# Performance work log

Hardware: AMD Instinct MI355X
Metric: run time of the kernel (lower is better)

The kernel has to match this reference:

```python
import jax, jax.numpy as jnp
import numpy as np

B, L, DM = 1, 512, 768
DS, DC, EX = 64, 4, 2
DI = EX * DM            # d_inner = 1536
DR = DM // 16           # dt_rank = 48


def setup_inputs() -> dict:
    key = jax.random.key(0)
    ks = jax.random.split(key, 12)
    s = 0.02
    inp = {
        "x": jax.random.normal(ks[0], (B, L, DM), dtype=jnp.float32),
        "ln_w": jnp.ones((DM,), jnp.float32),
        "ln_b": jnp.zeros((DM,), jnp.float32),
        "in_proj_w": jax.random.normal(ks[1], (2 * DI, DM), jnp.float32) * s,
        "conv_w": jax.random.normal(ks[2], (DI, 1, DC), jnp.float32) * s,
        "conv_b": jnp.zeros((DI,), jnp.float32),
        "x_proj_w": jax.random.normal(ks[3], (DR + 2 * DS, DI), jnp.float32) * s,
        "dt_proj_w": jax.random.normal(ks[4], (DI, DR), jnp.float32) * s,
        "dt_proj_b": jax.random.normal(ks[5], (DI,), jnp.float32) * s,
        "A_log": jnp.log(jnp.broadcast_to(jnp.arange(1, DS + 1, dtype=jnp.float32), (DI, DS))),
        "D": jnp.ones((DI,), jnp.float32),
        "out_proj_w": jax.random.normal(ks[6], (DM, DI), jnp.float32) * s,
    }
    return inp


def _layernorm(x, w, b, eps=1e-5):
    mu = jnp.mean(x, axis=-1, keepdims=True)
    var = jnp.mean((x - mu) ** 2, axis=-1, keepdims=True)
    return (x - mu) * jax.lax.rsqrt(var + eps) * w + b


def _causal_depthwise_conv(x, w, b):
    # x: [B, L, DI] -> conv over time, depthwise, causal (left pad DC-1)
    xc = jnp.transpose(x, (0, 2, 1))  # [B, DI, L]
    y = jax.lax.conv_general_dilated(
        xc, w, window_strides=(1,), padding=[(DC - 1, 0)],
        dimension_numbers=("NCH", "OIH", "NCH"), feature_group_count=DI)
    y = y + b[None, :, None]
    return jnp.transpose(y, (0, 2, 1))  # [B, L, DI]


def _selective_scan(deltaA, deltaB_u, C):
    # deltaA, deltaB_u: [B, L, DI, DS]; C: [B, L, DS]
    dA = jnp.transpose(deltaA, (1, 0, 2, 3))
    dBu = jnp.transpose(deltaB_u, (1, 0, 2, 3))
    Ct = jnp.transpose(C, (1, 0, 2))
    s0 = jnp.zeros(deltaA.shape[:1] + deltaA.shape[2:], deltaA.dtype).transpose(0, 1, 2)
    s0 = jnp.zeros((deltaA.shape[0], deltaA.shape[2], deltaA.shape[3]), deltaA.dtype)

    def step(s, inp):
        dA_t, dBu_t, C_t = inp
        s = dA_t * s + dBu_t                      # [B, DI, DS]
        y = jnp.einsum("bdn,bn->bd", s, C_t)      # [B, DI]
        return s, y

    _, ys = jax.lax.scan(step, s0, (dA, dBu, Ct))
    return jnp.transpose(ys, (1, 0, 2))           # [B, L, DI]


def reference(x, ln_w, ln_b, in_proj_w, conv_w, conv_b, x_proj_w,
              dt_proj_w, dt_proj_b, A_log, D, out_proj_w):
    residual = x
    h = _layernorm(x, ln_w, ln_b)
    xz = jnp.einsum("bld,ed->ble", h, in_proj_w)  # [B, L, 2*DI]
    x_in, z = jnp.split(xz, 2, axis=-1)
    x_in = jax.nn.silu(_causal_depthwise_conv(x_in, conv_w, conv_b))
    x_dbl = jnp.einsum("bld,ed->ble", x_in, x_proj_w)  # [B, L, DR+2*DS]
    dt, Bm, Cm = jnp.split(x_dbl, [DR, DR + DS], axis=-1)
    dt = jax.nn.softplus(jnp.einsum("blr,dr->bld", dt, dt_proj_w) + dt_proj_b)  # [B,L,DI]
    A = -jnp.exp(A_log)                                 # [DI, DS]
    deltaA = jnp.exp(dt[..., None] * A)                 # [B, L, DI, DS]
    deltaB_u = dt[..., None] * Bm[:, :, None, :] * x_in[..., None]
    y = _selective_scan(deltaA, deltaB_u, Cm)           # [B, L, DI]
    y = y + x_in * D
    y = y * jax.nn.silu(z)
    out = jnp.einsum("bld,ed->ble", y, out_proj_w)      # [B, L, DM]
    return residual + out
```

## Files before the change

### kernel.cpp

```cpp
#include <hip/hip_runtime.h>
#include <hip/hip_bf16.h>
#include <math.h>

#define L_SEQ 512
#define DM 768
#define DI 1536
#define DS 64
#define DC 4
#define DR 48
#define NXD 176
#define NC 8
#define TC 64

typedef __attribute__((ext_vector_type(8))) short short8;
typedef __attribute__((ext_vector_type(4))) float float4v;

#define NWI (2 * DI * DM)
#define NWX (NXD * DI)
#define NWDT (DI * DR)
#define NWO (DM * DI)
#define NXZ (L_SEQ * 2 * DI)
#define NXDBL (L_SEQ * NXD)
#define NXR (L_SEQ * DM)

#define B_LN 512
#define B_WI (NWI / 1024)
#define B_WX (NWX / 1024)
#define B_WDT (NWDT / 1024)
#define B_WO (NWO / 1024)
#define PREP_GRID (B_LN + B_WI + B_WX + B_WDT + B_WO)

__device__ __forceinline__ float bp_add(float p, int addr) {
  return p + __int_as_float(__builtin_amdgcn_ds_bpermute(addr, __float_as_int(p)));
}
__device__ __forceinline__ float lane_read(float v, int t) {
  return __int_as_float(__builtin_amdgcn_readlane(__float_as_int(v), t));
}
__device__ __forceinline__ short f2bf(float v) {
  __hip_bfloat16 h = __float2bfloat16(v);
  return *reinterpret_cast<short*>(&h);
}
__device__ __forceinline__ short8 cvt8f(const float* p, bool valid) {
  float4 u = *(const float4*)(p);
  float4 v = *(const float4*)(p + 4);
  short8 r;
  r[0] = f2bf(u.x); r[1] = f2bf(u.y); r[2] = f2bf(u.z); r[3] = f2bf(u.w);
  r[4] = f2bf(v.x); r[5] = f2bf(v.y); r[6] = f2bf(v.z); r[7] = f2bf(v.w);
  if (!valid) r = (short8)0;
  return r;
}

__device__ __forceinline__ void cvt_blk(const float* __restrict__ s,
                                        short* __restrict__ d, int b) {
  int i = b * 1024 + threadIdx.x * 4;
  float4 v = *(const float4*)(s + i);
  short4 o; o.x = f2bf(v.x); o.y = f2bf(v.y); o.z = f2bf(v.z); o.w = f2bf(v.w);
  *(short4*)(d + i) = o;
}
__global__ __launch_bounds__(256) void prep(
    const float* __restrict__ x, const float* __restrict__ lnw,
    const float* __restrict__ lnb, short* __restrict__ h,
    const float* __restrict__ wi, short* __restrict__ wib,
    const float* __restrict__ wx, short* __restrict__ wxb,
    const float* __restrict__ wdt, short* __restrict__ wdtb,
    const float* __restrict__ wo, short* __restrict__ wob) {
  int b = blockIdx.x;
  if (b < B_LN) {
    int l = b, tid = threadIdx.x;
    const float* xr = x + l * DM;
    float s = 0.f, s2 = 0.f;
    for (int i = tid; i < DM; i += 256) { float t = xr[i]; s += t; s2 += t * t; }
#pragma unroll
    for (int off = 32; off; off >>= 1) { s += __shfl_xor(s, off); s2 += __shfl_xor(s2, off); }
    __shared__ float ls[4], ls2[4];
    int wid = tid >> 6, lane = tid & 63;
    if (lane == 0) { ls[wid] = s; ls2[wid] = s2; }
    __syncthreads();
    s = ls[0] + ls[1] + ls[2] + ls[3];
    s2 = ls2[0] + ls2[1] + ls2[2] + ls2[3];
    float mean = s * (1.f / DM);
    float var = s2 * (1.f / DM) - mean * mean;
    float rstd = rsqrtf(var + 1e-5f);
    for (int i = tid; i < DM; i += 256)
      h[l * DM + i] = f2bf((xr[i] - mean) * rstd * lnw[i] + lnb[i]);
    return;
  }
  b -= B_LN;
  if (b < B_WI) { cvt_blk(wi, wib, b); return; }
  b -= B_WI;
  if (b < B_WX) { cvt_blk(wx, wxb, b); return; }
  b -= B_WX;
  if (b < B_WDT) { cvt_blk(wdt, wdtb, b); return; }
  b -= B_WDT;
  cvt_blk(wo, wob, b);
}

__global__ __launch_bounds__(256) void gemm_bf16(const short* __restrict__ A, int lda,
                                                 const short* __restrict__ B,
                                                 float* __restrict__ C,
                                                 int N, int K,
                                                 const float* __restrict__ res,
                                                 int mode) {
  int lane = threadIdx.x & 63, w = threadIdx.x >> 6;
  int fr = lane & 15, koff = (lane >> 4) * 8;
  int mbase = blockIdx.y * 64 + (w & 1) * 32;
  int nbase = blockIdx.x * 64 + (w >> 1) * 32;
  int kchunk = K / gridDim.z;
  int kbeg = blockIdx.z * kchunk;
  int nr0 = nbase + fr;      if (nr0 > N - 1) nr0 = N - 1;
  int nr1 = nbase + 16 + fr; if (nr1 > N - 1) nr1 = N - 1;
  const short* pA0 = A + (size_t)(mbase + fr) * lda + koff + kbeg;
  const short* pA1 = pA0 + (size_t)16 * lda;
  const short* pB0 = B + (size_t)nr0 * K + koff + kbeg;
  const short* pB1 = B + (size_t)nr1 * K + koff + kbeg;
  float4v acc00 = (float4v){0.f,0.f,0.f,0.f}, acc01 = acc00;
  float4v acc10 = acc00, acc11 = acc00;
  short8 a0A = *(const short8*)(pA0);      short8 a1A = *(const short8*)(pA1);
  short8 b0A = *(const short8*)(pB0);      short8 b1A = *(const short8*)(pB1);
  short8 a0B = *(const short8*)(pA0 + 32); short8 a1B = *(const short8*)(pA1 + 32);
  short8 b0B = *(const short8*)(pB0 + 32); short8 b1B = *(const short8*)(pB1 + 32);
  for (int k0 = 0; k0 < kchunk; k0 += 64) {
    short8 ca0 = a0A, ca1 = a1A, cb0 = b0A, cb1 = b1A;
    short8 da0 = a0B, da1 = a1B, db0 = b0B, db1 = b1B;
    int nA = k0 + 64; if (nA >= kchunk) nA = 0;
    int nB = k0 + 96; if (nB >= kchunk) nB = 32;
    a0A = *(const short8*)(pA0 + nA); a1A = *(const short8*)(pA1 + nA);
    b0A = *(const short8*)(pB0 + nA); b1A = *(const short8*)(pB1 + nA);
    a0B = *(const short8*)(pA0 + nB); a1B = *(const short8*)(pA1 + nB);
    b0B = *(const short8*)(pB0 + nB); b1B = *(const short8*)(pB1 + nB);
    acc00 = __builtin_amdgcn_mfma_f32_16x16x32_bf16(ca0, cb0, acc00, 0, 0, 0);
    acc01 = __builtin_amdgcn_mfma_f32_16x16x32_bf16(ca0, cb1, acc01, 0, 0, 0);
    acc10 = __builtin_amdgcn_mfma_f32_16x16x32_bf16(ca1, cb0, acc10, 0, 0, 0);
    acc11 = __builtin_amdgcn_mfma_f32_16x16x32_bf16(ca1, cb1, acc11, 0, 0, 0);
    acc00 = __builtin_amdgcn_mfma_f32_16x16x32_bf16(da0, db0, acc00, 0, 0, 0);
    acc01 = __builtin_amdgcn_mfma_f32_16x16x32_bf16(da0, db1, acc01, 0, 0, 0);
    acc10 = __builtin_amdgcn_mfma_f32_16x16x32_bf16(da1, db0, acc10, 0, 0, 0);
    acc11 = __builtin_amdgcn_mfma_f32_16x16x32_bf16(da1, db1, acc11, 0, 0, 0);
  }
  float* Cz = C + (size_t)blockIdx.z * (size_t)L_SEQ * (size_t)N;
  int col0 = nbase + fr, col1 = nbase + 16 + fr;
  int rb = mbase + (lane >> 4) * 4;
#pragma unroll
  for (int r = 0; r < 4; ++r) {
    size_t o00 = (size_t)(rb + r) * N;
    size_t o10 = (size_t)(rb + 16 + r) * N;
    if (col0 < N) {
      float v0 = acc00[r], v1 = acc10[r];
      if (mode == 2) { v0 += res[o00 + col0]; v1 += res[o10 + col0]; }
      Cz[o00 + col0] = v0; Cz[o10 + col0] = v1;
    }
    if (col1 < N) {
      float v0 = acc01[r], v1 = acc11[r];
      if (mode == 2) { v0 += res[o00 + col1]; v1 += res[o10 + col1]; }
      Cz[o00 + col1] = v0; Cz[o10 + col1] = v1;
    }
  }
}

__global__ __launch_bounds__(256) void reduce_add(const float* __restrict__ part,
                                                  int MN, int splitk,
                                                  float* __restrict__ out) {
  int i = blockIdx.x * 256 + threadIdx.x;
  if (i >= MN) return;
  float a = 0.f;
  for (int z = 0; z < splitk; ++z) a += part[(size_t)z * MN + i];
  out[i] = a;
}

__global__ __launch_bounds__(256) void dtp_gemm(const float* __restrict__ Axd,
                                                const short* __restrict__ Bw,
                                                float* __restrict__ dt,
                                                const float* __restrict__ bias) {
  int lane = threadIdx.x & 63, w = threadIdx.x >> 6;
  int fr = lane & 15, koff = (lane >> 4) * 8;
  int mbase = blockIdx.y * 64 + (w & 1) * 32;
  int nbase = blockIdx.x * 64 + (w >> 1) * 32;
  const float* pA0 = Axd + (size_t)(mbase + fr) * NXD;
  const float* pA1 = pA0 + (size_t)16 * NXD;
  const short* pB0 = Bw + (size_t)(nbase + fr) * DR;
  const short* pB1 = Bw + (size_t)(nbase + 16 + fr) * DR;
  float4v acc00 = (float4v){0.f,0.f,0.f,0.f}, acc01 = acc00;
  float4v acc10 = acc00, acc11 = acc00;
#pragma unroll
  for (int k0 = 0; k0 < 64; k0 += 32) {
    bool valid = (k0 + koff) < DR;
    int off = valid ? k0 + koff : 0;
    short8 a0 = cvt8f(pA0 + off, valid);
    short8 a1 = cvt8f(pA1 + off, valid);
    short8 b0 = *(const short8*)(pB0 + off);
    short8 b1 = *(const short8*)(pB1 + off);
    if (!valid) { b0 = (short8)0; b1 = (short8)0; }
    acc00 = __builtin_amdgcn_mfma_f32_16x16x32_bf16(a0, b0, acc00, 0, 0, 0);
    acc01 = __builtin_amdgcn_mfma_f32_16x16x32_bf16(a0, b1, acc01, 0, 0, 0);
    acc10 = __builtin_amdgcn_mfma_f32_16x16x32_bf16(a1, b0, acc10, 0, 0, 0);
    acc11 = __builtin_amdgcn_mfma_f32_16x16x32_bf16(a1, b1, acc11, 0, 0, 0);
  }
  int col0 = nbase + fr, col1 = nbase + 16 + fr;
  float bi0 = bias[col0], bi1 = bias[col1];
  int rb = mbase + (lane >> 4) * 4;
#pragma unroll
  for (int r = 0; r < 4; ++r) {
    float v0 = acc00[r] + bi0, v1 = acc01[r] + bi1;
    float v2 = acc10[r] + bi0, v3 = acc11[r] + bi1;
    v0 = (v0 > 20.f) ? v0 : log1pf(__expf(v0));
    v1 = (v1 > 20.f) ? v1 : log1pf(__expf(v1));
    v2 = (v2 > 20.f) ? v2 : log1pf(__expf(v2));
    v3 = (v3 > 20.f) ? v3 : log1pf(__expf(v3));
    dt[(size_t)(rb + r) * DI + col0] = v0;
    dt[(size_t)(rb + r) * DI + col1] = v1;
    dt[(size_t)(rb + 16 + r) * DI + col0] = v2;
    dt[(size_t)(rb + 16 + r) * DI + col1] = v3;
  }
}

__global__ __launch_bounds__(256) void conv_silu_kernel(const float* __restrict__ xz,
                                                        const float* __restrict__ cw,
                                                        const float* __restrict__ cb,
                                                        float* __restrict__ xc,
                                                        short* __restrict__ xcb) {
  int idx = blockIdx.x * 256 + threadIdx.x;
  if (idx >= L_SEQ * DI) return;
  int l = idx / DI, d = idx - l * DI;
  float acc = cb[d];
#pragma unroll
  for (int j = 0; j < DC; ++j) {
    int ll = l - (DC - 1) + j;
    if (ll >= 0) acc = fmaf(xz[(size_t)ll * (2 * DI) + d], cw[d * DC + j], acc);
  }
  float sig = 1.f / (1.f + __expf(-acc));
  float v = acc * sig;
  xc[idx] = v;
  xcb[idx] = f2bf(v);
}

__global__ __launch_bounds__(256) void scan_p1(const float* __restrict__ dt,
                                               const float* __restrict__ xc,
                                               const float* __restrict__ xdbl,
                                               const float* __restrict__ A_log,
                                               float* __restrict__ send,
                                               float* __restrict__ dts) {
  int lane = threadIdx.x & 63;
  int wid = threadIdx.x >> 6;
  int pair = blockIdx.x * 4 + wid;
  int c = __builtin_amdgcn_readfirstlane(pair / DI);
  int d = __builtin_amdgcn_readfirstlane(pair - (pair / DI) * DI);
  float A = -__expf(A_log[(size_t)d * DS + lane]);
  int l0 = c * TC;
  float dtv = dt[(size_t)(l0 + lane) * DI + d];
  float xv  = xc[(size_t)(l0 + lane) * DI + d];
  const float* pB = xdbl + (size_t)l0 * NXD + DR + lane;
  float s = 0.f;
#pragma unroll 8
  for (int t = 0; t < TC; ++t) {
    float dt_c = lane_read(dtv, t);
    float x_c  = lane_read(xv, t);
    float B_c  = pB[(size_t)t * NXD];
    float dA = __expf(dt_c * A);
    s = fmaf(dA, s, dt_c * x_c * B_c);
  }
  float dsum = dtv;
  dsum = bp_add(dsum, (lane ^ 1) << 2);  dsum = bp_add(dsum, (lane ^ 2) << 2);
  dsum = bp_add(dsum, (lane ^ 4) << 2);  dsum = bp_add(dsum, (lane ^ 8) << 2);
  dsum = bp_add(dsum, (lane ^ 16) << 2); dsum = bp_add(dsum, (lane ^ 32) << 2);
  send[((size_t)c * DI + d) * DS + lane] = s;
  if (lane == 0) dts[c * DI + d] = dsum;
}

__global__ __launch_bounds__(256) void scan_p2(const float* __restrict__ send,
                                               const float* __restrict__ dts,
                                               const float* __restrict__ A_log,
                                               float* __restrict__ sinit) {
  int lane = threadIdx.x & 63;
  int wid = threadIdx.x >> 6;
  int d = __builtin_amdgcn_readfirstlane(blockIdx.x * 4 + wid);
  float A = -__expf(A_log[(size_t)d * DS + lane]);
  float s = 0.f;
  for (int c = 1; c < NC; ++c) {
    float P = __expf(A * dts[(c - 1) * DI + d]);
    s = fmaf(P, s, send[((size_t)(c - 1) * DI + d) * DS + lane]);
    sinit[((size_t)c * DI + d) * DS + lane] = s;
  }
}

__global__ __launch_bounds__(256) void scan_p3(const float* __restrict__ dt,
                                               const float* __restrict__ xc,
                                               const float* __restrict__ xdbl,
                                               const float* __restrict__ A_log,
                                               const float* __restrict__ Dv,
                                               const float* __restrict__ xz,
                                               const float* __restrict__ sinit,
                                               short* __restrict__ y) {
  __shared__ float Pb[4][16][66];
  int lane = threadIdx.x & 63;
  int wid = threadIdx.x >> 6;
  int pair = blockIdx.x * 4 + wid;
  int c = __builtin_amdgcn_readfirstlane(pair / DI);
  int d = __builtin_amdgcn_readfirstlane(pair - (pair / DI) * DI);
  float A = -__expf(A_log[(size_t)d * DS + lane]);
  float Dd = Dv[d];
  int l0 = c * TC;
  float dtv = dt[(size_t)(l0 + lane) * DI + d];
  float xv  = xc[(size_t)(l0 + lane) * DI + d];
  float zv  = xz[(size_t)(l0 + lane) * (2 * DI) + DI + d];
  float s = (c == 0) ? 0.f : sinit[((size_t)c * DI + d) * DS + lane];
  const float* pB = xdbl + (size_t)l0 * NXD + DR + lane;
  float yv = 0.f;
#pragma unroll
  for (int sb = 0; sb < 4; ++sb) {
    float P[16];
#pragma unroll
    for (int j = 0; j < 16; ++j) {
      int t = sb * 16 + j;
      float dt_c = lane_read(dtv, t);
      float x_c  = lane_read(xv, t);
      float B_c  = pB[(size_t)t * NXD];
      float C_c  = pB[(size_t)t * NXD + DS];
      float dA = __expf(dt_c * A);
      s = fmaf(dA, s, dt_c * x_c * B_c);
      P[j] = s * C_c;
    }
#pragma unroll
    for (int j = 0; j < 16; ++j) Pb[wid][j][lane] = P[j];
    int t4 = lane >> 2, q = lane & 3;
    const float* row = &Pb[wid][t4][q * 16];
    float part = 0.f;
#pragma unroll
    for (int k = 0; k < 8; ++k) {
      float2 v2 = *(const float2*)(row + 2 * k);
      part += v2.x + v2.y;
    }
    part = bp_add(part, (lane ^ 1) << 2);
    part = bp_add(part, (lane ^ 2) << 2);
    float got = __int_as_float(
        __builtin_amdgcn_ds_bpermute((lane & 15) << 4, __float_as_int(part)));
    yv = ((lane >> 4) == sb) ? got : yv;
  }
  float sig = 1.f / (1.f + __expf(-zv));
  y[(size_t)(l0 + lane) * DI + d] = f2bf((yv + xv * Dd) * (zv * sig));
}

extern "C" void kernel_launch(void* const* d_in, const int* in_sizes, int n_in,
                              void* d_out, int out_size, void* d_ws, size_t ws_size,
                              hipStream_t stream) {
  const float* x         = (const float*)d_in[0];
  const float* ln_w      = (const float*)d_in[1];
  const float* ln_b      = (const float*)d_in[2];
  const float* in_proj_w = (const float*)d_in[3];
  const float* conv_w    = (const float*)d_in[4];
  const float* conv_b    = (const float*)d_in[5];
  const float* x_proj_w  = (const float*)d_in[6];
  const float* dt_proj_w = (const float*)d_in[7];
  const float* dt_proj_b = (const float*)d_in[8];
  const float* A_log     = (const float*)d_in[9];
  const float* Dv        = (const float*)d_in[10];
  const float* out_proj_w= (const float*)d_in[11];
  float* out = (float*)d_out;

  float* ws = (float*)d_ws;
  float* xz    = ws;
  float* xconv = xz + NXZ;
  float* xdbl  = xconv + 786432;
  float* dtb   = xdbl + NXDBL;
  float* send  = dtb + 786432;
  float* dts   = send + 688128;
  float* sinit = dts + 10752;
  float* part2 = sinit + 786432;
  float* fend  = part2 + 720896;
  short* h_bf   = (short*)fend;
  short* wi_bf  = h_bf + NXR;
  short* wx_bf  = wi_bf + NWI;
  short* wdt_bf = wx_bf + NWX;
  short* wo_bf  = wdt_bf + NWDT;
  short* xc_bf  = wo_bf + NWO;
  short* y_bf   = xc_bf + (L_SEQ * DI);

  prep<<<PREP_GRID, 256, 0, stream>>>(x, ln_w, ln_b, h_bf,
                                      in_proj_w, wi_bf, x_proj_w, wx_bf,
                                      dt_proj_w, wdt_bf, out_proj_w, wo_bf);

  gemm_bf16<<<dim3(2 * DI / 64, L_SEQ / 64, 1), 256, 0, stream>>>(
      h_bf, DM, wi_bf, xz, 2 * DI, DM, nullptr, 0);

  conv_silu_kernel<<<(L_SEQ * DI) / 256, 256, 0, stream>>>(xz, conv_w, conv_b,
                                                           xconv, xc_bf);

  gemm_bf16<<<dim3((NXD + 63) / 64, L_SEQ / 64, 8), 256, 0, stream>>>(
      xc_bf, DI, wx_bf, part2, NXD, DI, nullptr, 0);
  reduce_add<<<(NXDBL + 255) / 256, 256, 0, stream>>>(part2, NXDBL, 8, xdbl);

  dtp_gemm<<<dim3(DI / 64, L_SEQ / 64), 256, 0, stream>>>(
      xdbl, wdt_bf, dtb, dt_proj_b);

  scan_p1<<<((NC - 1) * DI) / 4, 256, 0, stream>>>(dtb, xconv, xdbl, A_log, send, dts);
  scan_p2<<<DI / 4, 256, 0, stream>>>(send, dts, A_log, sinit);
  scan_p3<<<(NC * DI) / 4, 256, 0, stream>>>(dtb, xconv, xdbl, A_log, Dv, xz, sinit, y_bf);

  gemm_bf16<<<dim3(DM / 64, L_SEQ / 64, 1), 256, 0, stream>>>(
      y_bf, DI, wo_bf, out, DM, DI, x, 2);
}
```

Baseline: 212.4 us.

## Fuse all stages into one cooperative persistent kernel with grid syncs

Replaces the chain of separate kernel launches (prep, three GEMMs, conv, reduce, dt projection, three scan phases) with one cooperative kernel of 512 blocks that runs each stage in turn, separated by grid-wide barriers. The split-K x_proj GEMM now accumulates straight into a zeroed xdbl buffer with atomic adds, so the separate partial buffer and reduce kernel are gone. The aim is to remove launch gaps and the extra partial-sum traffic. In exchange, stages that used more than 512 blocks now loop over work, several stages leave most blocks idle, grid.sync adds its own barrier cost, and atomic accumulation makes the float sums order-dependent.

```diff
diff --git a/kernel.cpp b/kernel.cpp
--- a/kernel.cpp
+++ b/kernel.cpp
@@ -1,6 +1,9 @@
 #include <hip/hip_runtime.h>
+#include <hip/hip_cooperative_groups.h>
 #include <hip/hip_bf16.h>
 #include <math.h>
+
+namespace cg = cooperative_groups;
 
 #define L_SEQ 512
 #define DM 768
@@ -23,12 +26,22 @@
 #define NXDBL (L_SEQ * NXD)
 #define NXR (L_SEQ * DM)
 
-#define B_LN 512
-#define B_WI (NWI / 1024)
-#define B_WX (NWX / 1024)
-#define B_WDT (NWDT / 1024)
-#define B_WO (NWO / 1024)
-#define PREP_GRID (B_LN + B_WI + B_WX + B_WDT + B_WO)
+#define J_LN 512
+#define J_WI (NWI / 1024)
+#define J_WX (NWX / 1024)
+#define J_WDT (NWDT / 1024)
+#define J_WO (NWO / 1024)
+#define J_ZXD (NXDBL / 1024)
+#define NJOBS (J_LN + J_WI + J_WX + J_WDT + J_WO + J_ZXD)
+
+#define GRID_BLOCKS 512
+
+struct Params {
+  const float *x, *lnw, *lnb, *wi, *conv_w, *conv_b, *wx, *wdt, *dt_b, *A_log, *Dv, *wo;
+  float *out;
+  float *xz, *xconv, *xdbl, *dtb, *send, *dts, *sinit;
+  short *h_bf, *wi_bf, *wx_bf, *wdt_bf, *wo_bf, *xc_bf, *y_bf;
+};
 
 __device__ __forceinline__ float bp_add(float p, int addr) {
   return p + __int_as_float(__builtin_amdgcn_ds_bpermute(addr, __float_as_int(p)));
@@ -49,7 +62,9 @@
   if (!valid) r = (short8)0;
   return r;
 }
-
+__device__ __forceinline__ void atomic_addf(float* p, float v) {
+  __hip_atomic_fetch_add(p, v, __ATOMIC_RELAXED, __HIP_MEMORY_SCOPE_AGENT);
+}
 __device__ __forceinline__ void cvt_blk(const float* __restrict__ s,
                                         short* __restrict__ d, int b) {
   int i = b * 1024 + threadIdx.x * 4;
@@ -57,62 +72,22 @@
   short4 o; o.x = f2bf(v.x); o.y = f2bf(v.y); o.z = f2bf(v.z); o.w = f2bf(v.w);
   *(short4*)(d + i) = o;
 }
-__global__ __launch_bounds__(256) void prep(
-    const float* __restrict__ x, const float* __restrict__ lnw,
-    const float* __restrict__ lnb, short* __restrict__ h,
-    const float* __restrict__ wi, short* __restrict__ wib,
-    const float* __restrict__ wx, short* __restrict__ wxb,
-    const float* __restrict__ wdt, short* __restrict__ wdtb,
-    const float* __restrict__ wo, short* __restrict__ wob) {
-  int b = blockIdx.x;
-  if (b < B_LN) {
-    int l = b, tid = threadIdx.x;
-    const float* xr = x + l * DM;
-    float s = 0.f, s2 = 0.f;
-    for (int i = tid; i < DM; i += 256) { float t = xr[i]; s += t; s2 += t * t; }
-#pragma unroll
-    for (int off = 32; off; off >>= 1) { s += __shfl_xor(s, off); s2 += __shfl_xor(s2, off); }
-    __shared__ float ls[4], ls2[4];
-    int wid = tid >> 6, lane = tid & 63;
-    if (lane == 0) { ls[wid] = s; ls2[wid] = s2; }
-    __syncthreads();
-    s = ls[0] + ls[1] + ls[2] + ls[3];
-    s2 = ls2[0] + ls2[1] + ls2[2] + ls2[3];
-    float mean = s * (1.f / DM);
-    float var = s2 * (1.f / DM) - mean * mean;
-    float rstd = rsqrtf(var + 1e-5f);
-    for (int i = tid; i < DM; i += 256)
-      h[l * DM + i] = f2bf((xr[i] - mean) * rstd * lnw[i] + lnb[i]);
-    return;
-  }
-  b -= B_LN;
-  if (b < B_WI) { cvt_blk(wi, wib, b); return; }
-  b -= B_WI;
-  if (b < B_WX) { cvt_blk(wx, wxb, b); return; }
-  b -= B_WX;
-  if (b < B_WDT) { cvt_blk(wdt, wdtb, b); return; }
-  b -= B_WDT;
-  cvt_blk(wo, wob, b);
-}
-
-__global__ __launch_bounds__(256) void gemm_bf16(const short* __restrict__ A, int lda,
-                                                 const short* __restrict__ B,
-                                                 float* __restrict__ C,
-                                                 int N, int K,
-                                                 const float* __restrict__ res,
-                                                 int mode) {
-  int lane = threadIdx.x & 63, w = threadIdx.x >> 6;
+
+__device__ __forceinline__ void gemm_tile(const short* A, int lda,
+                                          const short* B, int ldb,
+                                          float* C, int N,
+                                          int kbeg, int kchunk,
+                                          const float* res, int mode,
+                                          int bx, int by, int lane, int w) {
   int fr = lane & 15, koff = (lane >> 4) * 8;
-  int mbase = blockIdx.y * 64 + (w & 1) * 32;
-  int nbase = blockIdx.x * 64 + (w >> 1) * 32;
-  int kchunk = K / gridDim.z;
-  int kbeg = blockIdx.z * kchunk;
+  int mbase = by * 64 + (w & 1) * 32;
+  int nbase = bx * 64 + (w >> 1) * 32;
   int nr0 = nbase + fr;      if (nr0 > N - 1) nr0 = N - 1;
   int nr1 = nbase + 16 + fr; if (nr1 > N - 1) nr1 = N - 1;
   const short* pA0 = A + (size_t)(mbase + fr) * lda + koff + kbeg;
   const short* pA1 = pA0 + (size_t)16 * lda;
-  const short* pB0 = B + (size_t)nr0 * K + koff + kbeg;
-  const short* pB1 = B + (size_t)nr1 * K + koff + kbeg;
+  const short* pB0 = B + (size_t)nr0 * ldb + koff + kbeg;
+  const short* pB1 = B + (size_t)nr1 * ldb + koff + kbeg;
   float4v acc00 = (float4v){0.f,0.f,0.f,0.f}, acc01 = acc00;
   float4v acc10 = acc00, acc11 = acc00;
   short8 a0A = *(const short8*)(pA0);      short8 a1A = *(const short8*)(pA1);
@@ -137,7 +112,6 @@
     acc10 = __builtin_amdgcn_mfma_f32_16x16x32_bf16(da1, db0, acc10, 0, 0, 0);
     acc11 = __builtin_amdgcn_mfma_f32_16x16x32_bf16(da1, db1, acc11, 0, 0, 0);
   }
-  float* Cz = C + (size_t)blockIdx.z * (size_t)L_SEQ * (size_t)N;
   int col0 = nbase + fr, col1 = nbase + 16 + fr;
   int rb = mbase + (lane >> 4) * 4;
 #pragma unroll
@@ -145,36 +119,34 @@
     size_t o00 = (size_t)(rb + r) * N;
     size_t o10 = (size_t)(rb + 16 + r) * N;
     if (col0 < N) {
-      float v0 = acc00[r], v1 = acc10[r];
-      if (mode == 2) { v0 += res[o00 + col0]; v1 += res[o10 + col0]; }
-      Cz[o00 + col0] = v0; Cz[o10 + col0] = v1;
+      if (mode == 1) {
+        atomic_addf(&C[o00 + col0], acc00[r]);
+        atomic_addf(&C[o10 + col0], acc10[r]);
+      } else {
+        float v0 = acc00[r], v1 = acc10[r];
+        if (mode == 2) { v0 += res[o00 + col0]; v1 += res[o10 + col0]; }
+        C[o00 + col0] = v0; C[o10 + col0] = v1;
+      }
     }
     if (col1 < N) {
-      float v0 = acc01[r], v1 = acc11[r];
-      if (mode == 2) { v0 += res[o00 + col1]; v1 += res[o10 + col1]; }
-      Cz[o00 + col1] = v0; Cz[o10 + col1] = v1;
-    }
-  }
-}
-
-__global__ __launch_bounds__(256) void reduce_add(const float* __restrict__ part,
-                                                  int MN, int splitk,
-                                                  float* __restrict__ out) {
-  int i = blockIdx.x * 256 + threadIdx.x;
-  if (i >= MN) return;
-  float a = 0.f;
-  for (int z = 0; z < splitk; ++z) a += part[(size_t)z * MN + i];
-  out[i] = a;
-}
-
-__global__ __launch_bounds__(256) void dtp_gemm(const float* __restrict__ Axd,
-                                                const short* __restrict__ Bw,
-                                                float* __restrict__ dt,
-                                                const float* __restrict__ bias) {
-  int lane = threadIdx.x & 63, w = threadIdx.x >> 6;
+      if (mode == 1) {
+        atomic_addf(&C[o00 + col1], acc01[r]);
+        atomic_addf(&C[o10 + col1], acc11[r]);
+      } else {
+        float v0 = acc01[r], v1 = acc11[r];
+        if (mode == 2) { v0 += res[o00 + col1]; v1 += res[o10 + col1]; }
+        C[o00 + col1] = v0; C[o10 + col1] = v1;
+      }
+    }
+  }
+}
+
+__device__ __forceinline__ void dtp_tile(const float* Axd, const short* Bw,
+                                         float* dt, const float* bias,
+                                         int bx, int by, int lane, int w) {
   int fr = lane & 15, koff = (lane >> 4) * 8;
-  int mbase = blockIdx.y * 64 + (w & 1) * 32;
-  int nbase = blockIdx.x * 64 + (w >> 1) * 32;
+  int mbase = by * 64 + (w & 1) * 32;
+  int nbase = bx * 64 + (w >> 1) * 32;
   const float* pA0 = Axd + (size_t)(mbase + fr) * NXD;
   const float* pA1 = pA0 + (size_t)16 * NXD;
   const short* pB0 = Bw + (size_t)(nbase + fr) * DR;
@@ -213,188 +185,207 @@
   }
 }
 
-__global__ __launch_bounds__(256) void conv_silu_kernel(const float* __restrict__ xz,
-                                                        const float* __restrict__ cw,
-                                                        const float* __restrict__ cb,
-                                                        float* __restrict__ xc,
-                                                        short* __restrict__ xcb) {
-  int idx = blockIdx.x * 256 + threadIdx.x;
-  if (idx >= L_SEQ * DI) return;
-  int l = idx / DI, d = idx - l * DI;
-  float acc = cb[d];
-#pragma unroll
-  for (int j = 0; j < DC; ++j) {
-    int ll = l - (DC - 1) + j;
-    if (ll >= 0) acc = fmaf(xz[(size_t)ll * (2 * DI) + d], cw[d * DC + j], acc);
-  }
-  float sig = 1.f / (1.f + __expf(-acc));
-  float v = acc * sig;
-  xc[idx] = v;
-  xcb[idx] = f2bf(v);
-}
-
-__global__ __launch_bounds__(256) void scan_p1(const float* __restrict__ dt,
-                                               const float* __restrict__ xc,
-                                               const float* __restrict__ xdbl,
-                                               const float* __restrict__ A_log,
-                                               float* __restrict__ send,
-                                               float* __restrict__ dts) {
-  int lane = threadIdx.x & 63;
-  int wid = threadIdx.x >> 6;
-  int pair = blockIdx.x * 4 + wid;
-  int c = __builtin_amdgcn_readfirstlane(pair / DI);
-  int d = __builtin_amdgcn_readfirstlane(pair - (pair / DI) * DI);
-  float A = -__expf(A_log[(size_t)d * DS + lane]);
-  int l0 = c * TC;
-  float dtv = dt[(size_t)(l0 + lane) * DI + d];
-  float xv  = xc[(size_t)(l0 + lane) * DI + d];
-  const float* pB = xdbl + (size_t)l0 * NXD + DR + lane;
-  float s = 0.f;
+__global__ __launch_bounds__(256, 2) void mamba_mega(Params p) {
+  cg::grid_group grid = cg::this_grid();
+  const int tid = threadIdx.x;
+  const int lane = tid & 63, wid = tid >> 6;
+  const int gb = blockIdx.x;
+  __shared__ float Pb[4][16][66];
+  __shared__ float ls[4], ls2[4];
+
+  for (int job = gb; job < NJOBS; job += GRID_BLOCKS) {
+    if (job < J_LN) {
+      int l = job;
+      const float* xr = p.x + l * DM;
+      float s = 0.f, s2 = 0.f;
+      for (int i = tid; i < DM; i += 256) { float t = xr[i]; s += t; s2 += t * t; }
+#pragma unroll
+      for (int off = 32; off; off >>= 1) { s += __shfl_xor(s, off); s2 += __shfl_xor(s2, off); }
+      if (lane == 0) { ls[wid] = s; ls2[wid] = s2; }
+      __syncthreads();
+      s = ls[0] + ls[1] + ls[2] + ls[3];
+      s2 = ls2[0] + ls2[1] + ls2[2] + ls2[3];
+      __syncthreads();
+      float mean = s * (1.f / DM);
+      float var = s2 * (1.f / DM) - mean * mean;
+      float rstd = rsqrtf(var + 1e-5f);
+      for (int i = tid; i < DM; i += 256)
+        p.h_bf[l * DM + i] = f2bf((xr[i] - mean) * rstd * p.lnw[i] + p.lnb[i]);
+      continue;
+    }
+    int b = job - J_LN;
+    if (b < J_WI) { cvt_blk(p.wi, p.wi_bf, b); continue; }
+    b -= J_WI;
+    if (b < J_WX) { cvt_blk(p.wx, p.wx_bf, b); continue; }
+    b -= J_WX;
+    if (b < J_WDT) { cvt_blk(p.wdt, p.wdt_bf, b); continue; }
+    b -= J_WDT;
+    if (b < J_WO) { cvt_blk(p.wo, p.wo_bf, b); continue; }
+    b -= J_WO;
+    { int i = b * 1024 + tid * 4; *(float4*)(p.xdbl + i) = make_float4(0.f, 0.f, 0.f, 0.f); }
+  }
+  grid.sync();
+
+  if (gb < 384)
+    gemm_tile(p.h_bf, DM, p.wi_bf, DM, p.xz, 2 * DI, 0, DM, nullptr, 0,
+              gb % 48, gb / 48, lane, wid);
+  grid.sync();
+
+  for (int blk = gb; blk < (L_SEQ * DI) / 256; blk += GRID_BLOCKS) {
+    int idx = blk * 256 + tid;
+    int l = idx / DI, d = idx - l * DI;
+    float acc = p.conv_b[d];
+#pragma unroll
+    for (int j = 0; j < DC; ++j) {
+      int ll = l - (DC - 1) + j;
+      if (ll >= 0) acc = fmaf(p.xz[(size_t)ll * (2 * DI) + d], p.conv_w[d * DC + j], acc);
+    }
+    float sig = 1.f / (1.f + __expf(-acc));
+    float v = acc * sig;
+    p.xconv[idx] = v;
+    p.xc_bf[idx] = f2bf(v);
+  }
+  grid.sync();
+
+  if (gb < 192) {
+    int bx = gb % 3, by = (gb / 3) % 8, bz = gb / 24;
+    gemm_tile(p.xc_bf, DI, p.wx_bf, DI, p.xdbl, NXD, bz * 192, 192, nullptr, 1,
+              bx, by, lane, wid);
+  }
+  grid.sync();
+
+  if (gb < 192)
+    dtp_tile(p.xdbl, p.wdt_bf, p.dtb, p.dt_b, gb % 24, gb / 24, lane, wid);
+  grid.sync();
+
+  for (int g = gb; g < ((NC - 1) * DI) / 4; g += GRID_BLOCKS) {
+    int pair = g * 4 + wid;
+    int c = __builtin_amdgcn_readfirstlane(pair / DI);
+    int d = __builtin_amdgcn_readfirstlane(pair - (pair / DI) * DI);
+    float A = -__expf(p.A_log[(size_t)d * DS + lane]);
+    int l0 = c * TC;
+    float dtv = p.dtb[(size_t)(l0 + lane) * DI + d];
+    float xv  = p.xconv[(size_t)(l0 + lane) * DI + d];
+    const float* pB = p.xdbl + (size_t)l0 * NXD + DR + lane;
+    float s = 0.f;
 #pragma unroll 8
-  for (int t = 0; t < TC; ++t) {
-    float dt_c = lane_read(dtv, t);
-    float x_c  = lane_read(xv, t);
-    float B_c  = pB[(size_t)t * NXD];
-    float dA = __expf(dt_c * A);
-    s = fmaf(dA, s, dt_c * x_c * B_c);
-  }
-  float dsum = dtv;
-  dsum = bp_add(dsum, (lane ^ 1) << 2);  dsum = bp_add(dsum, (lane ^ 2) << 2);
-  dsum = bp_add(dsum, (lane ^ 4) << 2);  dsum = bp_add(dsum, (lane ^ 8) << 2);
-  dsum = bp_add(dsum, (lane ^ 16) << 2); dsum = bp_add(dsum, (lane ^ 32) << 2);
-  send[((size_t)c * DI + d) * DS + lane] = s;
-  if (lane == 0) dts[c * DI + d] = dsum;
-}
-
-__global__ __launch_bounds__(256) void scan_p2(const float* __restrict__ send,
-                                               const float* __restrict__ dts,
-                                               const float* __restrict__ A_log,
-                                               float* __restrict__ sinit) {
-  int lane = threadIdx.x & 63;
-  int wid = threadIdx.x >> 6;
-  int d = __builtin_amdgcn_readfirstlane(blockIdx.x * 4 + wid);
-  float A = -__expf(A_log[(size_t)d * DS + lane]);
-  float s = 0.f;
-  for (int c = 1; c < NC; ++c) {
-    float P = __expf(A * dts[(c - 1) * DI + d]);
-    s = fmaf(P, s, send[((size_t)(c - 1) * DI + d) * DS + lane]);
-    sinit[((size_t)c * DI + d) * DS + lane] = s;
-  }
-}
-
-__global__ __launch_bounds__(256) void scan_p3(const float* __restrict__ dt,
-                                               const float* __restrict__ xc,
-                                               const float* __restrict__ xdbl,
-                                               const float* __restrict__ A_log,
-                                               const float* __restrict__ Dv,
-                                               const float* __restrict__ xz,
-                                               const float* __restrict__ sinit,
-                                               short* __restrict__ y) {
-  __shared__ float Pb[4][16][66];
-  int lane = threadIdx.x & 63;
-  int wid = threadIdx.x >> 6;
-  int pair = blockIdx.x * 4 + wid;
-  int c = __builtin_amdgcn_readfirstlane(pair / DI);
-  int d = __builtin_amdgcn_readfirstlane(pair - (pair / DI) * DI);
-  float A = -__expf(A_log[(size_t)d * DS + lane]);
-  float Dd = Dv[d];
-  int l0 = c * TC;
-  float dtv = dt[(size_t)(l0 + lane) * DI + d];
-  float xv  = xc[(size_t)(l0 + lane) * DI + d];
-  float zv  = xz[(size_t)(l0 + lane) * (2 * DI) + DI + d];
-  float s = (c == 0) ? 0.f : sinit[((size_t)c * DI + d) * DS + lane];
-  const float* pB = xdbl + (size_t)l0 * NXD + DR + lane;
-  float yv = 0.f;
-#pragma unroll
-  for (int sb = 0; sb < 4; ++sb) {
-    float P[16];
-#pragma unroll
-    for (int j = 0; j < 16; ++j) {
-      int t = sb * 16 + j;
+    for (int t = 0; t < TC; ++t) {
       float dt_c = lane_read(dtv, t);
       float x_c  = lane_read(xv, t);
       float B_c  = pB[(size_t)t * NXD];
-      float C_c  = pB[(size_t)t * NXD + DS];
       float dA = __expf(dt_c * A);
       s = fmaf(dA, s, dt_c * x_c * B_c);
-      P[j] = s * C_c;
-    }
-#pragma unroll
-    for (int j = 0; j < 16; ++j) Pb[wid][j][lane] = P[j];
-    int t4 = lane >> 2, q = lane & 3;
-    const float* row = &Pb[wid][t4][q * 16];
-    float part = 0.f;
-#pragma unroll
-    for (int k = 0; k < 8; ++k) {
-      float2 v2 = *(const float2*)(row + 2 * k);
-      part += v2.x + v2.y;
-    }
-    part = bp_add(part, (lane ^ 1) << 2);
-    part = bp_add(part, (lane ^ 2) << 2);
-    float got = __int_as_float(
-        __builtin_amdgcn_ds_bpermute((lane & 15) << 4, __float_as_int(part)));
-    yv = ((lane >> 4) == sb) ? got : yv;
-  }
-  float sig = 1.f / (1.f + __expf(-zv));
-  y[(size_t)(l0 + lane) * DI + d] = f2bf((yv + xv * Dd) * (zv * sig));
+    }
+    float dsum = dtv;
+    dsum = bp_add(dsum, (lane ^ 1) << 2);  dsum = bp_add(dsum, (lane ^ 2) << 2);
+    dsum = bp_add(dsum, (lane ^ 4) << 2);  dsum = bp_add(dsum, (lane ^ 8) << 2);
+    dsum = bp_add(dsum, (lane ^ 16) << 2); dsum = bp_add(dsum, (lane ^ 32) << 2);
+    p.send[((size_t)c * DI + d) * DS + lane] = s;
+    if (lane == 0) p.dts[c * DI + d] = dsum;
+  }
+  grid.sync();
+
+  if (gb < DI / 4) {
+    int d = __builtin_amdgcn_readfirstlane(gb * 4 + wid);
+    float A = -__expf(p.A_log[(size_t)d * DS + lane]);
+    float s = 0.f;
+    for (int c = 1; c < NC; ++c) {
+      float P = __expf(A * p.dts[(c - 1) * DI + d]);
+      s = fmaf(P, s, p.send[((size_t)(c - 1) * DI + d) * DS + lane]);
+      p.sinit[((size_t)c * DI + d) * DS + lane] = s;
+    }
+  }
+  grid.sync();
+
+  for (int g = gb; g < (NC * DI) / 4; g += GRID_BLOCKS) {
+    int pair = g * 4 + wid;
+    int c = __builtin_amdgcn_readfirstlane(pair / DI);
+    int d = __builtin_amdgcn_readfirstlane(pair - (pair / DI) * DI);
+    float A = -__expf(p.A_log[(size_t)d * DS + lane]);
+    float Dd = p.Dv[d];
+    int l0 = c * TC;
+    float dtv = p.dtb[(size_t)(l0 + lane) * DI + d];
+    float xv  = p.xconv[(size_t)(l0 + lane) * DI + d];
+    float zv  = p.xz[(size_t)(l0 + lane) * (2 * DI) + DI + d];
+    float s = (c == 0) ? 0.f : p.sinit[((size_t)c * DI + d) * DS + lane];
+    const float* pB = p.xdbl + (size_t)l0 * NXD + DR + lane;
+    float yv = 0.f;
+#pragma unroll
+    for (int sb = 0; sb < 4; ++sb) {
+      float P[16];
+#pragma unroll
+      for (int j = 0; j < 16; ++j) {
+        int t = sb * 16 + j;
+        float dt_c = lane_read(dtv, t);
+        float x_c  = lane_read(xv, t);
+        float B_c  = pB[(size_t)t * NXD];
+        float C_c  = pB[(size_t)t * NXD + DS];
+        float dA = __expf(dt_c * A);
+        s = fmaf(dA, s, dt_c * x_c * B_c);
+        P[j] = s * C_c;
+      }
+#pragma unroll
+      for (int j = 0; j < 16; ++j) Pb[wid][j][lane] = P[j];
+      int t4 = lane >> 2, q = lane & 3;
+      const float* row = &Pb[wid][t4][q * 16];
+      float part = 0.f;
+#pragma unroll
+      for (int k = 0; k < 8; ++k) {
+        float2 v2 = *(const float2*)(row + 2 * k);
+        part += v2.x + v2.y;
+      }
+      part = bp_add(part, (lane ^ 1) << 2);
+      part = bp_add(part, (lane ^ 2) << 2);
+      float got = __int_as_float(
+          __builtin_amdgcn_ds_bpermute((lane & 15) << 4, __float_as_int(part)));
+      yv = ((lane >> 4) == sb) ? got : yv;
+    }
+    float sig = 1.f / (1.f + __expf(-zv));
+    p.y_bf[(size_t)(l0 + lane) * DI + d] = f2bf((yv + xv * Dd) * (zv * sig));
+  }
+  grid.sync();
+
+  if (gb < 96)
+    gemm_tile(p.y_bf, DI, p.wo_bf, DI, p.out, DM, 0, DI, p.x, 2,
+              gb % 12, gb / 12, lane, wid);
 }
 
 extern "C" void kernel_launch(void* const* d_in, const int* in_sizes, int n_in,
                               void* d_out, int out_size, void* d_ws, size_t ws_size,
                               hipStream_t stream) {
-  const float* x         = (const float*)d_in[0];
-  const float* ln_w      = (const float*)d_in[1];
-  const float* ln_b      = (const float*)d_in[2];
-  const float* in_proj_w = (const float*)d_in[3];
-  const float* conv_w    = (const float*)d_in[4];
-  const float* conv_b    = (const float*)d_in[5];
-  const float* x_proj_w  = (const float*)d_in[6];
-  const float* dt_proj_w = (const float*)d_in[7];
-  const float* dt_proj_b = (const float*)d_in[8];
-  const float* A_log     = (const float*)d_in[9];
-  const float* Dv        = (const float*)d_in[10];
-  const float* out_proj_w= (const float*)d_in[11];
-  float* out = (float*)d_out;
+  Params p;
+  p.x      = (const float*)d_in[0];
+  p.lnw    = (const float*)d_in[1];
+  p.lnb    = (const float*)d_in[2];
+  p.wi     = (const float*)d_in[3];
+  p.conv_w = (const float*)d_in[4];
+  p.conv_b = (const float*)d_in[5];
+  p.wx     = (const float*)d_in[6];
+  p.wdt    = (const float*)d_in[7];
+  p.dt_b   = (const float*)d_in[8];
+  p.A_log  = (const float*)d_in[9];
+  p.Dv     = (const float*)d_in[10];
+  p.wo     = (const float*)d_in[11];
+  p.out    = (float*)d_out;
 
   float* ws = (float*)d_ws;
-  float* xz    = ws;
-  float* xconv = xz + NXZ;
-  float* xdbl  = xconv + 786432;
-  float* dtb   = xdbl + NXDBL;
-  float* send  = dtb + 786432;
-  float* dts   = send + 688128;
-  float* sinit = dts + 10752;
-  float* part2 = sinit + 786432;
-  float* fend  = part2 + 720896;
-  short* h_bf   = (short*)fend;
-  short* wi_bf  = h_bf + NXR;
-  short* wx_bf  = wi_bf + NWI;
-  short* wdt_bf = wx_bf + NWX;
-  short* wo_bf  = wdt_bf + NWDT;
-  short* xc_bf  = wo_bf + NWO;
-  short* y_bf   = xc_bf + (L_SEQ * DI);
-
-  prep<<<PREP_GRID, 256, 0, stream>>>(x, ln_w, ln_b, h_bf,
-                                      in_proj_w, wi_bf, x_proj_w, wx_bf,
-                                      dt_proj_w, wdt_bf, out_proj_w, wo_bf);
-
-  gemm_bf16<<<dim3(2 * DI / 64, L_SEQ / 64, 1), 256, 0, stream>>>(
-      h_bf, DM, wi_bf, xz, 2 * DI, DM, nullptr, 0);
-
-  conv_silu_kernel<<<(L_SEQ * DI) / 256, 256, 0, stream>>>(xz, conv_w, conv_b,
-                                                           xconv, xc_bf);
-
-  gemm_bf16<<<dim3((NXD + 63) / 64, L_SEQ / 64, 8), 256, 0, stream>>>(
-      xc_bf, DI, wx_bf, part2, NXD, DI, nullptr, 0);
-  reduce_add<<<(NXDBL + 255) / 256, 256, 0, stream>>>(part2, NXDBL, 8, xdbl);
-
-  dtp_gemm<<<dim3(DI / 64, L_SEQ / 64), 256, 0, stream>>>(
-      xdbl, wdt_bf, dtb, dt_proj_b);
-
-  scan_p1<<<((NC - 1) * DI) / 4, 256, 0, stream>>>(dtb, xconv, xdbl, A_log, send, dts);
-  scan_p2<<<DI / 4, 256, 0, stream>>>(send, dts, A_log, sinit);
-  scan_p3<<<(NC * DI) / 4, 256, 0, stream>>>(dtb, xconv, xdbl, A_log, Dv, xz, sinit, y_bf);
-
-  gemm_bf16<<<dim3(DM / 64, L_SEQ / 64, 1), 256, 0, stream>>>(
-      y_bf, DI, wo_bf, out, DM, DI, x, 2);
-}
+  p.xz    = ws;
+  p.xconv = p.xz + NXZ;
+  p.xdbl  = p.xconv + L_SEQ*DI;
+  p.dtb   = p.xdbl + NXDBL;
+  p.send  = p.dtb + L_SEQ*DI;
+  p.dts   = p.send + 688128;
+  p.sinit = p.dts + 10752;
+  float* fend = p.sinit + 786432;
+  p.h_bf   = (short*)fend;
+  p.wi_bf  = p.h_bf + NXR;
+  p.wx_bf  = p.wi_bf + NWI;
+  p.wdt_bf = p.wx_bf + NWX;
+  p.wo_bf  = p.wdt_bf + NWDT;
+  p.xc_bf  = p.wo_bf + NWO;
+  p.y_bf   = p.xc_bf + L_SEQ*DI;
+
+  void* args[] = { (void*)&p };
+  hipLaunchCooperativeKernel((const void*)mamba_mega, dim3(GRID_BLOCKS),
+                             dim3(256), args, 0, stream);
+}
```

New measurement: 698.0 us. +228.6%, slower.
